# Kernel tuning notes

Measured on AMD Instinct MI355X. Metric: run time of the kernel, lower is better.

Reference implementation:

```python
import jax, jax.numpy as jnp
import numpy as np
import math

FACTOR = 5

def setup_inputs() -> dict:
    key = jax.random.key(0)
    k1, k2, k3, k4 = jax.random.split(key, 4)
    B, L, H, D = 4, 4096, 8, 64
    sample_k = min(FACTOR * int(np.ceil(np.log(L))), L)  # 45
    return {
        "queries": jax.random.normal(k1, (B, L, H, D), dtype=jnp.float32),
        "keys": jax.random.normal(k2, (B, L, H, D), dtype=jnp.float32),
        "values": jax.random.normal(k3, (B, L, H, D), dtype=jnp.float32),
        "index_sample": jax.random.randint(k4, (L, sample_k), 0, L, dtype=jnp.int64),
    }

def reference(queries, keys, values, index_sample):
    # [B, L, H, D] -> [B, H, L, D]
    Q = jnp.transpose(queries, (0, 2, 1, 3))
    K = jnp.transpose(keys, (0, 2, 1, 3))
    V = jnp.transpose(values, (0, 2, 1, 3))
    b, h, l_q, d = Q.shape
    l_k = K.shape[2]

    # n_top (u) per Informer: factor * ceil(ln(l_q)), capped at l_q
    u = min(FACTOR * int(math.ceil(math.log(l_q))), l_q)

    # --- _prob_QK: sampled QK scores ---
    # K_sample: [b, h, l_q, sample_k, d] via shared per-query random sample
    K_sample = K[:, :, index_sample, :]
    # Q_K_sample: [b, h, l_q, sample_k]
    Q_K_sample = jnp.einsum("bhqd,bhqsd->bhqs", Q, K_sample)
    # sparsity measure M: max - mean(sum/l_k)
    M = Q_K_sample.max(axis=-1) - Q_K_sample.sum(axis=-1) / l_k
    # top-u queries (indices; order irrelevant to the math)
    _, M_top = jax.lax.top_k(M, u)  # [b, h, u]

    # Q_reduce: [b, h, u, d]
    Q_reduce = jnp.take_along_axis(Q, M_top[..., None], axis=2)
    # full scores for selected queries: [b, h, u, l_k]
    scale = 1.0 / math.sqrt(d)
    scores_top = jnp.einsum("bhud,bhkd->bhuk", Q_reduce, K) * scale

    # --- initial context: mean of V broadcast over queries ---
    context = jnp.broadcast_to(V.mean(axis=2, keepdims=True), (b, h, l_q, d))

    # --- update context at selected query positions ---
    attn = jax.nn.softmax(scores_top, axis=-1)          # [b, h, u, l_k]
    upd = jnp.einsum("bhuk,bhkd->bhud", attn, V)         # [b, h, u, d]
    bi = jnp.arange(b)[:, None, None]
    hi = jnp.arange(h)[None, :, None]
    context = context.at[bi, hi, M_top].set(upd)

    # [B, H, L, D] -> [B, L, H, D]
    return jnp.transpose(context, (0, 2, 1, 3))
```

## Files before the change

kernel.cpp:

```cpp
#include <hip/hip_runtime.h>
#include <stdint.h>

#define B_ 4
#define L_ 4096
#define H_ 8
#define D_ 64
#define S_ 45
#define U_ 45
#define BH_ 32
#define KC_ 16
#define STRIDE_ (H_*D_)
#define BSTR_ ((size_t)L_*H_*D_)

__device__ __forceinline__ bool detect_idx64(const int* idxp){
    bool z = true;
    #pragma unroll
    for (int i = 1; i < 32; i += 2) z = z && (idxp[i] == 0);
    return z;
}

__global__ __launch_bounds__(256) void kM(const float* __restrict__ Qb,
                                          const float* __restrict__ Kb,
                                          const int* __restrict__ idxp,
                                          float* __restrict__ Mout){
    int g = blockIdx.x;
    int xcd  = g & 7;
    int slot = g >> 3;
    int bh   = xcd*4 + (slot >> 6);
    int chunk= slot & 63;
    int b = bh >> 3, h = bh & 7;
    int q0 = chunk * 64;
    bool idx64 = detect_idx64(idxp);

    __shared__ float qs[64][64];
    for (int i = threadIdx.x; i < 64*16; i += 256){
        int qrow = i >> 4, c = i & 15;
        float4 v = ((const float4*)(Qb + (size_t)b*BSTR_ + (size_t)(q0+qrow)*STRIDE_ + h*D_))[c];
        *(float4*)&qs[qrow][c*4] = v;
    }
    __syncthreads();

    int lane8 = threadIdx.x & 7;
    const float* kbase = Kb + (size_t)b*BSTR_ + h*D_;

    for (int qq = 0; qq < 2; qq++){
        int qrow = (threadIdx.x >> 3) + 32*qq;
        int qg   = q0 + qrow;
        float4 qf0 = *(const float4*)&qs[qrow][lane8*4];
        float4 qf1 = *(const float4*)&qs[qrow][lane8*4 + 32];
        float mx = -1e30f, sm = 0.f;
        #pragma unroll 3
        for (int s = 0; s < S_; s++){
            int flat = qg * S_ + s;
            int ki = idx64 ? idxp[2*flat] : idxp[flat];
            const float* kr = kbase + (size_t)ki*STRIDE_;
            float4 k0 = *(const float4*)(kr + lane8*4);
            float4 k1 = *(const float4*)(kr + lane8*4 + 32);
            float a0 = qf0.x*k0.x;
            a0 = fmaf(qf0.y, k0.y, a0);
            a0 = fmaf(qf0.z, k0.z, a0);
            a0 = fmaf(qf0.w, k0.w, a0);
            float a1 = qf1.x*k1.x;
            a1 = fmaf(qf1.y, k1.y, a1);
            a1 = fmaf(qf1.z, k1.z, a1);
            a1 = fmaf(qf1.w, k1.w, a1);
            float p = a0 + a1;
            p += __shfl_xor(p, 1);
            p += __shfl_xor(p, 2);
            p += __shfl_xor(p, 4);
            mx = fmaxf(mx, p); sm += p;
        }
        if (lane8 == 0) Mout[bh * L_ + qg] = mx - sm * (1.0f / L_);
    }
}

__global__ __launch_bounds__(512) void kTopF(const float* __restrict__ M,
                                             int* __restrict__ Mtop,
                                             float* __restrict__ meanZ,
                                             int* __restrict__ selRow){
    int bh = blockIdx.x;
    int t = threadIdx.x;
    if (t < 64) meanZ[bh*64 + t] = 0.f;
    for (int j = t; j < L_; j += 512) selRow[(size_t)bh*L_ + j] = 0;

    __shared__ float cV[8*U_];
    __shared__ int   cI[8*U_];
    int wv = t >> 6, lane = t & 63;
    const float* Mr = M + (size_t)bh*L_ + wv*512;
    float v[8];
    #pragma unroll
    for (int j = 0; j < 8; j++) v[j] = Mr[lane + 64*j];

    for (int it = 0; it < U_; it++){
        float best = -1e30f; int bidx = 0x7fffffff;
        #pragma unroll
        for (int j = 0; j < 8; j++){
            int id = lane + 64*j;
            if (v[j] > best){ best = v[j]; bidx = id; }
        }
        #pragma unroll
        for (int off = 1; off < 64; off <<= 1){
            float ov = __shfl_xor(best, off); int oi = __shfl_xor(bidx, off);
            if (ov > best || (ov == best && oi < bidx)){ best = ov; bidx = oi; }
        }
        if (lane == 0){ cV[wv*U_ + it] = best; cI[wv*U_ + it] = wv*512 + bidx; }
        if (lane == (bidx & 63)) v[bidx >> 6] = -1e30f;
    }
    __syncthreads();
    if (t < 64){
        float v2[6]; int id2[6];
        #pragma unroll
        for (int j = 0; j < 6; j++){
            int slot = t + 64*j;
            if (slot < 8*U_){ v2[j] = cV[slot]; id2[j] = cI[slot]; }
            else            { v2[j] = -1e30f;  id2[j] = 0x7fffffff; }
        }
        for (int it = 0; it < U_; it++){
            float best = -1e30f; int bidx = 0x7fffffff; int bj = 0;
            #pragma unroll
            for (int j = 0; j < 6; j++){
                if (v2[j] > best || (v2[j] == best && id2[j] < bidx)){
                    best = v2[j]; bidx = id2[j]; bj = j;
                }
            }
            float myBest = best; int myIdx = bidx;
            #pragma unroll
            for (int off = 1; off < 64; off <<= 1){
                float ov = __shfl_xor(best, off); int oi = __shfl_xor(bidx, off);
                if (ov > best || (ov == best && oi < bidx)){ best = ov; bidx = oi; }
            }
            if (t == 0){
                Mtop[bh*U_ + it] = bidx;
                selRow[(size_t)bh*L_ + bidx] = it + 1;
            }
            if (myBest == best && myIdx == bidx) v2[bj] = -1e30f;
        }
    }
}

__global__ __launch_bounds__(256) void kAttnPart(const float* __restrict__ Qb,
                                                 const float* __restrict__ Kb,
                                                 const float* __restrict__ Vb,
                                                 const int*   __restrict__ Mtop,
                                                 float* __restrict__ Opart,
                                                 float* __restrict__ mlG,
                                                 float* __restrict__ mean){
    int bh = blockIdx.y, b = bh >> 3, h = bh & 7;
    int kc = blockIdx.x, uh = blockIdx.z;
    int u0 = uh ? 23 : 0;
    int nu = uh ? 22 : 23;
    int t = threadIdx.x;
    __shared__ float S[24][260];
    __shared__ float red[4][8][64];
    __shared__ int   qidx[23];

    if (t < nu) qidx[t] = Mtop[bh*U_ + u0 + t];
    __syncthreads();

    int k = kc*256 + t;
    float4 kf[16];
    const float4* K4 = (const float4*)(Kb + (size_t)b*BSTR_ + (size_t)k*STRIDE_ + h*D_);
    #pragma unroll
    for (int c = 0; c < 16; c++) kf[c] = K4[c];
    for (int u = 0; u < nu; u++){
        int qi = __builtin_amdgcn_readfirstlane(qidx[u]);
        const float4* qp = (const float4*)(Qb + (size_t)b*BSTR_ + (size_t)qi*STRIDE_ + h*D_);
        float a0=0.f, a1=0.f, a2=0.f, a3=0.f;
        #pragma unroll
        for (int c = 0; c < 16; c++){
            float4 qv = qp[c];
            a0 = fmaf(qv.x, kf[c].x, a0);
            a1 = fmaf(qv.y, kf[c].y, a1);
            a2 = fmaf(qv.z, kf[c].z, a2);
            a3 = fmaf(qv.w, kf[c].w, a3);
        }
        S[u][t] = ((a0+a1)+(a2+a3)) * 0.125f;
    }
    __syncthreads();

    int wv = t >> 6, lane = t & 63;
    for (int u = wv; u < nu; u += 4){
        float4 sv = *(const float4*)&S[u][lane*4];
        float m = fmaxf(fmaxf(sv.x, sv.y), fmaxf(sv.z, sv.w));
        #pragma unroll
        for (int off = 1; off < 64; off <<= 1) m = fmaxf(m, __shfl_xor(m, off));
        float e0 = __expf(sv.x - m), e1 = __expf(sv.y - m);
        float e2 = __expf(sv.z - m), e3 = __expf(sv.w - m);
        float ls = (e0+e1)+(e2+e3);
        #pragma unroll
        for (int off = 1; off < 64; off <<= 1) ls += __shfl_xor(ls, off);
        float4 pv; pv.x = e0; pv.y = e1; pv.z = e2; pv.w = e3;
        *(float4*)&S[u][lane*4] = pv;
        if (lane == 0){
            size_t mi = ((size_t)(bh*KC_ + kc)*U_ + u0 + u)*2;
            mlG[mi] = m; mlG[mi+1] = ls;
        }
    }
    __syncthreads();

    int d8 = t & 7, ks = t >> 3;
    float vsum[8];
    #pragma unroll
    for (int j = 0; j < 8; j++) vsum[j] = 0.f;
    for (int g = 0; g < 3; g++){
        int g0 = g*8; int nug = (nu - g0 < 8) ? (nu - g0) : 8;
        float acc[8][8];
        #pragma unroll
        for (int r = 0; r < 8; r++)
            #pragma unroll
            for (int j = 0; j < 8; j++) acc[r][j] = 0.f;
        for (int i = 0; i < 8; i++){
            int kk = ks + 32*i;
            const float4* V4 = (const float4*)(Vb + (size_t)b*BSTR_ +
                        (size_t)(kc*256 + kk)*STRIDE_ + h*D_);
            float4 va = V4[d8*2], vb = V4[d8*2+1];
            float vf[8] = {va.x, va.y, va.z, va.w, vb.x, vb.y, vb.z, vb.w};
            if (uh == 0 && g == 0){
                #pragma unroll
                for (int j = 0; j < 8; j++) vsum[j] += vf[j];
            }
            #pragma unroll
            for (int r = 0; r < 8; r++){
                float p = S[g0+r][kk];
                #pragma unroll
                for (int j = 0; j < 8; j++) acc[r][j] = fmaf(p, vf[j], acc[r][j]);
            }
        }
        #pragma unroll
        for (int off = 8; off <= 32; off <<= 1)
            #pragma unroll
            for (int r = 0; r < 8; r++)
                #pragma unroll
                for (int j = 0; j < 8; j++) acc[r][j] += __shfl_xor(acc[r][j], off);
        if (lane < 8){
            for (int r = 0; r < 8; r++)
                #pragma unroll
                for (int j = 0; j < 8; j++) red[wv][r][d8*8+j] = acc[r][j];
        }
        __syncthreads();
        for (int tt = t; tt < nug*64; tt += 256){
            int r = tt >> 6, d = tt & 63;
            float s = red[0][r][d] + red[1][r][d] + red[2][r][d] + red[3][r][d];
            Opart[((size_t)(bh*KC_ + kc)*U_ + u0 + g0 + r)*64 + d] = s;
        }
        __syncthreads();
    }
    if (uh == 0){
        #pragma unroll
        for (int off = 8; off <= 32; off <<= 1)
            #pragma unroll
            for (int j = 0; j < 8; j++) vsum[j] += __shfl_xor(vsum[j], off);
        if (lane < 8){
            #pragma unroll
            for (int j = 0; j < 8; j++) red[wv][0][lane*8 + j] = vsum[j];
        }
        __syncthreads();
        if (t < 64){
            float s = red[0][0][t] + red[1][0][t] + red[2][0][t] + red[3][0][t];
            atomicAdd(&mean[bh*64 + t], s);
        }
    }
}

__global__ __launch_bounds__(256) void kOut(const float* __restrict__ mean,
                                            const int*   __restrict__ selRow,
                                            const float* __restrict__ mlG,
                                            const float* __restrict__ Opart,
                                            float* __restrict__ out){
    size_t t = (size_t)blockIdx.x*256 + threadIdx.x;
    int d16 = (int)(t & 15); int h = (int)((t >> 4) & 7);
    int l   = (int)((t >> 7) & 4095); int b = (int)(t >> 19);
    int bh = b*8 + h;
    int sel = selRow[(size_t)bh*L_ + l];
    float4 o;
    if (sel == 0){
        o = *(const float4*)(mean + bh*64 + d16*4);
        const float inv = 1.0f / L_;
        o.x *= inv; o.y *= inv; o.z *= inv; o.w *= inv;
    } else {
        int u = sel - 1;
        float mstar = -1e30f;
        #pragma unroll
        for (int kc = 0; kc < KC_; kc++)
            mstar = fmaxf(mstar, mlG[((size_t)(bh*KC_ + kc)*U_ + u)*2]);
        float lsum = 0.f;
        float4 acc; acc.x = acc.y = acc.z = acc.w = 0.f;
        #pragma unroll
        for (int kc = 0; kc < KC_; kc++){
            size_t mi = ((size_t)(bh*KC_ + kc)*U_ + u)*2;
            float w = __expf(mlG[mi] - mstar);
            lsum = fmaf(mlG[mi+1], w, lsum);
            float4 op = *(const float4*)(Opart + ((size_t)(bh*KC_ + kc)*U_ + u)*64 + d16*4);
            acc.x = fmaf(w, op.x, acc.x);
            acc.y = fmaf(w, op.y, acc.y);
            acc.z = fmaf(w, op.z, acc.z);
            acc.w = fmaf(w, op.w, acc.w);
        }
        float inv = 1.0f / lsum;
        acc.x *= inv; acc.y *= inv; acc.z *= inv; acc.w *= inv;
        o = acc;
    }
    ((float4*)out)[t] = o;
}

extern "C" void kernel_launch(void* const* d_in, const int* in_sizes, int n_in,
                              void* d_out, int out_size, void* d_ws, size_t ws_size,
                              hipStream_t stream) {
    const float* Qb  = (const float*)d_in[0];
    const float* Kb  = (const float*)d_in[1];
    const float* Vb  = (const float*)d_in[2];
    const int*   idx = (const int*)d_in[3];
    float* out = (float*)d_out;

    float* ws = (float*)d_ws;
    float* M      = ws;
    int*   Mtop   = (int*)(ws + 131072);
    float* mean   = ws + 133120;
    int*   selRow = (int*)(ws + 135168);
    float* mlG    = ws + 266240;
    float* Opart  = ws + 315392;

    kM        <<<dim3(2048),       dim3(256), 0, stream>>>(Qb, Kb, idx, M);
    kTopF     <<<dim3(32),         dim3(512), 0, stream>>>(M, Mtop, mean, selRow);
    kAttnPart <<<dim3(KC_, 32, 2), dim3(256), 0, stream>>>(Qb, Kb, Vb, Mtop, Opart, mlG, mean);
    kOut      <<<dim3(8192),       dim3(256), 0, stream>>>(mean, selRow, mlG, Opart, out);
}
```

Baseline: 344.4 us.

## Restructure sampled-QK kernel to process four heads per query and share indices

```diff
diff --git a/kernel.cpp b/kernel.cpp
--- a/kernel.cpp
+++ b/kernel.cpp
@@ -24,53 +24,63 @@
                                           const int* __restrict__ idxp,
                                           float* __restrict__ Mout){
     int g = blockIdx.x;
-    int xcd  = g & 7;
-    int slot = g >> 3;
-    int bh   = xcd*4 + (slot >> 6);
-    int chunk= slot & 63;
-    int b = bh >> 3, h = bh & 7;
-    int q0 = chunk * 64;
+    int grp8 = g & 7;
+    int b  = grp8 >> 1;
+    int hg = grp8 & 1;
+    int chunk = g >> 3;
+    int q0 = chunk * 16;
     bool idx64 = detect_idx64(idxp);
 
-    __shared__ float qs[64][64];
-    for (int i = threadIdx.x; i < 64*16; i += 256){
-        int qrow = i >> 4, c = i & 15;
-        float4 v = ((const float4*)(Qb + (size_t)b*BSTR_ + (size_t)(q0+qrow)*STRIDE_ + h*D_))[c];
-        *(float4*)&qs[qrow][c*4] = v;
-    }
-    __syncthreads();
-
-    int lane8 = threadIdx.x & 7;
-    const float* kbase = Kb + (size_t)b*BSTR_ + h*D_;
-
-    for (int qq = 0; qq < 2; qq++){
-        int qrow = (threadIdx.x >> 3) + 32*qq;
-        int qg   = q0 + qrow;
-        float4 qf0 = *(const float4*)&qs[qrow][lane8*4];
-        float4 qf1 = *(const float4*)&qs[qrow][lane8*4 + 32];
-        float mx = -1e30f, sm = 0.f;
-        #pragma unroll 3
-        for (int s = 0; s < S_; s++){
-            int flat = qg * S_ + s;
-            int ki = idx64 ? idxp[2*flat] : idxp[flat];
-            const float* kr = kbase + (size_t)ki*STRIDE_;
-            float4 k0 = *(const float4*)(kr + lane8*4);
-            float4 k1 = *(const float4*)(kr + lane8*4 + 32);
-            float a0 = qf0.x*k0.x;
-            a0 = fmaf(qf0.y, k0.y, a0);
-            a0 = fmaf(qf0.z, k0.z, a0);
-            a0 = fmaf(qf0.w, k0.w, a0);
-            float a1 = qf1.x*k1.x;
-            a1 = fmaf(qf1.y, k1.y, a1);
-            a1 = fmaf(qf1.z, k1.z, a1);
-            a1 = fmaf(qf1.w, k1.w, a1);
-            float p = a0 + a1;
-            p += __shfl_xor(p, 1);
-            p += __shfl_xor(p, 2);
-            p += __shfl_xor(p, 4);
-            mx = fmaxf(mx, p); sm += p;
-        }
-        if (lane8 == 0) Mout[bh * L_ + qg] = mx - sm * (1.0f / L_);
+    __shared__ int lidx[16*S_];
+    for (int i = threadIdx.x; i < 16*S_; i += 256)
+        lidx[i] = idx64 ? idxp[2*(q0*S_ + i)] : idxp[q0*S_ + i];
+    __syncthreads();
+
+    int lane = threadIdx.x & 63;
+    int w    = threadIdx.x >> 6;
+    int grp  = lane >> 4;
+    int l16  = lane & 15;
+    int ql   = w*4 + grp;
+    int q    = q0 + ql;
+
+    const float4* qr = (const float4*)(Qb + (size_t)b*BSTR_ + (size_t)q*STRIDE_ + hg*256);
+    float4 qf0 = qr[l16];
+    float4 qf1 = qr[16 + l16];
+    float4 qf2 = qr[32 + l16];
+    float4 qf3 = qr[48 + l16];
+
+    const float* kbase = Kb + (size_t)b*BSTR_ + hg*256;
+    float mxa = -1e30f, mxb = -1e30f, sma = 0.f, smb = 0.f;
+    const int* myIdx = &lidx[ql*S_];
+
+    #pragma unroll 3
+    for (int s = 0; s < S_; s++){
+        int ki = myIdx[s];
+        const float4* kr = (const float4*)(kbase + (size_t)ki*STRIDE_);
+        float4 k0 = kr[l16], k1 = kr[16+l16], k2 = kr[32+l16], k3 = kr[48+l16];
+        float p0 = qf0.x*k0.x; p0 = fmaf(qf0.y,k0.y,p0); p0 = fmaf(qf0.z,k0.z,p0); p0 = fmaf(qf0.w,k0.w,p0);
+        float p1 = qf1.x*k1.x; p1 = fmaf(qf1.y,k1.y,p1); p1 = fmaf(qf1.z,k1.z,p1); p1 = fmaf(qf1.w,k1.w,p1);
+        float p2 = qf2.x*k2.x; p2 = fmaf(qf2.y,k2.y,p2); p2 = fmaf(qf2.z,k2.z,p2); p2 = fmaf(qf2.w,k2.w,p2);
+        float p3 = qf3.x*k3.x; p3 = fmaf(qf3.y,k3.y,p3); p3 = fmaf(qf3.z,k3.z,p3); p3 = fmaf(qf3.w,k3.w,p3);
+        float u0 = p0 + __shfl_xor(p0, 8);
+        float u1 = p1 + __shfl_xor(p1, 8);
+        float u2 = p2 + __shfl_xor(p2, 8);
+        float u3 = p3 + __shfl_xor(p3, 8);
+        float va = (l16 < 8) ? u0 : u2;
+        float vb = (l16 < 8) ? u1 : u3;
+        #pragma unroll
+        for (int off = 1; off < 8; off <<= 1){
+            va += __shfl_xor(va, off);
+            vb += __shfl_xor(vb, off);
+        }
+        mxa = fmaxf(mxa, va); sma += va;
+        mxb = fmaxf(mxb, vb); smb += vb;
+    }
+    int hsel = (l16==0) ? 0 : (l16==1) ? 1 : (l16==8) ? 2 : (l16==9) ? 3 : -1;
+    if (hsel >= 0){
+        float mv = (l16 & 1) ? mxb : mxa;
+        float sv = (l16 & 1) ? smb : sma;
+        Mout[(size_t)(b*8 + hg*4 + hsel)*L_ + q] = mv - sv*(1.0f/L_);
     }
 }
 
```

Measured after the change: 333.7 us. -3.1%, faster.
